# Performance work log

Hardware: AMD Instinct MI355X
Metric: run time of the kernel (lower is better)

The kernel has to match this reference:

```python
import jax, jax.numpy as jnp
import numpy as np

N_NODES = 50000
N_EDGES = 800000
D_IN = 64
D_OUT = 64
EPS = 0.0  # DGL GINConv default init_eps=0, not learnable


def setup_inputs() -> dict:
    key = jax.random.key(0)
    k1, k2, k3, k4, k5 = jax.random.split(key, 5)
    node_inputs = jax.random.normal(k1, (N_NODES, D_IN), dtype=jnp.float32)
    src = jax.random.randint(k2, (N_EDGES,), 0, N_NODES, dtype=jnp.int64)
    dst = jax.random.randint(k3, (N_EDGES,), 0, N_NODES, dtype=jnp.int64)
    # nn.Linear(in_feats, out_feats) params (PyTorch layout: W [out, in])
    bound = 1.0 / np.sqrt(D_IN)
    W = jax.random.uniform(k4, (D_OUT, D_IN), dtype=jnp.float32, minval=-bound, maxval=bound)
    b = jax.random.uniform(k5, (D_OUT,), dtype=jnp.float32, minval=-bound, maxval=bound)
    return {"node_inputs": node_inputs, "W": W, "b": b, "src": src, "dst": dst}


def reference(node_inputs, W, b, src, dst):
    # GIN sum aggregation: for each node, sum features of in-neighbors
    # messages: [E, D_IN] gathered, scatter-summed into [N, D_IN]
    agg = jax.ops.segment_sum(node_inputs[src], dst, num_segments=N_NODES)
    h = (1.0 + EPS) * node_inputs + agg          # [N, D_IN]
    h = h @ W.T + b                              # Linear -> [N, D_OUT]
    h = jnp.tanh(h)
    # Dropout is identity in eval mode (deterministic reference)
    return h
```

## Files before the change

kernel.cpp:

```cpp
#include <hip/hip_runtime.h>

#define N_NODES 50000
#define N_EDGES 800000
#define D 64

#define NBIN 512
#define BINW 98
#define PBLK 160
#define EPB  5000
#define CAPB 26
#define NCAP 64
#define WGROUP 260

typedef int iv4 __attribute__((ext_vector_type(4)));

__global__ __launch_bounds__(512) void gin_part(const int* __restrict__ src,
                                                const int* __restrict__ dst,
                                                unsigned int* __restrict__ regions,
                                                int* __restrict__ bincnt) {
    __shared__ int lcnt[NBIN];
    const int tid = threadIdx.x;
    if (tid < NBIN) lcnt[tid] = 0;
    __syncthreads();

    const int ebase = blockIdx.x * EPB;
    unsigned int* __restrict__ rbase = regions + (size_t)blockIdx.x * NBIN * CAPB;

    for (int i = tid; i < EPB / 4; i += 512) {
        const int e = ebase + i * 4;
        const iv4 d4 = *(const iv4*)&dst[e];
        const iv4 s4 = *(const iv4*)&src[e];
        const int dd[4] = {d4.x, d4.y, d4.z, d4.w};
        const int ss[4] = {s4.x, s4.y, s4.z, s4.w};
        #pragma unroll
        for (int j = 0; j < 4; ++j) {
            const int bin = dd[j] / BINW;
            const int pos = atomicAdd(&lcnt[bin], 1);
            if (pos < CAPB)
                rbase[bin * CAPB + pos] = ((unsigned)dd[j] << 16) | (unsigned)ss[j];
        }
    }
    __syncthreads();
    if (tid < NBIN) bincnt[blockIdx.x * NBIN + tid] = lcnt[tid] < CAPB ? lcnt[tid] : CAPB;
}

__device__ __forceinline__ float fast_tanh(float v) {
    return 1.0f - 2.0f / (__expf(2.0f * v) + 1.0f);
}

__global__ __launch_bounds__(1024) void gin_node(const float* __restrict__ x,
                                                 const float* __restrict__ W,
                                                 const float* __restrict__ bias,
                                                 const unsigned int* __restrict__ regions,
                                                 const int* __restrict__ bincnt,
                                                 float* __restrict__ out) {
    __shared__ unsigned short sbuck[BINW * NCAP];
    __shared__ int   lcnt[BINW];
    __shared__ float Wt2[16 * WGROUP];
    __shared__ float hs[16][68];

    const int tid  = threadIdx.x;
    const int lane = tid & 63;
    const int wv   = tid >> 6;
    const int b    = blockIdx.x;
    const int lo   = b * BINW;

    if (tid < BINW) lcnt[tid] = 0;
    #pragma unroll
    for (int i = tid; i < D * D; i += 1024) {
        const int f = i >> 6, k = i & 63;
        Wt2[(k >> 2) * WGROUP + (f << 2) + (k & 3)] = W[i];
    }
    __syncthreads();

    for (int pb = wv; pb < PBLK; pb += 16) {
        const int n = bincnt[pb * NBIN + b];
        if (lane < n) {
            const unsigned e = regions[((size_t)pb * NBIN + b) * CAPB + lane];
            const int dl  = (int)(e >> 16) - lo;
            const int pos = atomicAdd(&lcnt[dl], 1);
            if (pos < NCAP) sbuck[dl * NCAP + pos] = (unsigned short)(e & 0xffffu);
        }
    }
    __syncthreads();

    const float bf = bias[lane];
    for (int li = wv; li < BINW; li += 16) {
        const int node = lo + li;
        if (node >= N_NODES) break;
        int cn = lcnt[li]; if (cn > NCAP) cn = NCAP;
        const int sid = (int)sbuck[li * NCAP + lane];

        float a0 = x[(size_t)node * D + lane];
        float a1 = 0.f, a2 = 0.f, a3 = 0.f, a4 = 0.f, a5 = 0.f, a6 = 0.f, a7 = 0.f;
        for (int i = 0; i < cn; i += 8) {
            int i0 = __shfl(sid, i + 0), i1 = __shfl(sid, i + 1);
            int i2 = __shfl(sid, i + 2), i3 = __shfl(sid, i + 3);
            int i4 = __shfl(sid, i + 4), i5 = __shfl(sid, i + 5);
            int i6 = __shfl(sid, i + 6), i7 = __shfl(sid, i + 7);
            const int rem = cn - i;
            i0 = (0 < rem) ? i0 : 0;  i1 = (1 < rem) ? i1 : 0;
            i2 = (2 < rem) ? i2 : 0;  i3 = (3 < rem) ? i3 : 0;
            i4 = (4 < rem) ? i4 : 0;  i5 = (5 < rem) ? i5 : 0;
            i6 = (6 < rem) ? i6 : 0;  i7 = (7 < rem) ? i7 : 0;
            const float v0 = x[(size_t)i0 * D + lane], v1 = x[(size_t)i1 * D + lane];
            const float v2 = x[(size_t)i2 * D + lane], v3 = x[(size_t)i3 * D + lane];
            const float v4 = x[(size_t)i4 * D + lane], v5 = x[(size_t)i5 * D + lane];
            const float v6 = x[(size_t)i6 * D + lane], v7 = x[(size_t)i7 * D + lane];
            a0 += (0 < rem) ? v0 : 0.f;  a1 += (1 < rem) ? v1 : 0.f;
            a2 += (2 < rem) ? v2 : 0.f;  a3 += (3 < rem) ? v3 : 0.f;
            a4 += (4 < rem) ? v4 : 0.f;  a5 += (5 < rem) ? v5 : 0.f;
            a6 += (6 < rem) ? v6 : 0.f;  a7 += (7 < rem) ? v7 : 0.f;
        }
        hs[wv][lane] = ((a0 + a1) + (a2 + a3)) + ((a4 + a5) + (a6 + a7));

        float r0 = bf, r1 = 0.f, r2 = 0.f, r3 = 0.f;
        #pragma unroll
        for (int kg = 0; kg < 16; ++kg) {
            const float4 w  = *(const float4*)&Wt2[kg * WGROUP + (lane << 2)];
            const float4 hv = *(const float4*)&hs[wv][kg << 2];
            r0 += hv.x * w.x;
            r1 += hv.y * w.y;
            r2 += hv.z * w.z;
            r3 += hv.w * w.w;
        }
        out[(size_t)node * D + lane] = fast_tanh((r0 + r1) + (r2 + r3));
    }
}

extern "C" void kernel_launch(void* const* d_in, const int* in_sizes, int n_in,
                              void* d_out, int out_size, void* d_ws, size_t ws_size,
                              hipStream_t stream) {
    const float* x    = (const float*)d_in[0];
    const float* W    = (const float*)d_in[1];
    const float* bias = (const float*)d_in[2];
    const int*   src  = (const int*)d_in[3];
    const int*   dst  = (const int*)d_in[4];
    float*       out  = (float*)d_out;

    unsigned int* regions = (unsigned int*)d_ws;
    int*          bincnt  = (int*)(regions + (size_t)PBLK * NBIN * CAPB);

    gin_part<<<PBLK, 512, 0, stream>>>(src, dst, regions, bincnt);
    gin_node<<<NBIN, 1024, 0, stream>>>(x, W, bias, regions, bincnt, out);
}
```

Baseline: 125.9 us.

## Aggregate four nodes per wavefront with float4 gathers and pair partition reads

Each wavefront now handles four nodes at once, with 16 lanes per node gathering neighbour rows as float4 loads, reading source ids straight from LDS instead of through shuffles. Nodes are split into contiguous chunks per wave, and the following matvec loops over the four staged rows. The partition-read phase also lets each wave read two partition bins at once using 32-lane halves, since bins hold at most 26 entries. This widens per-lane loads and cuts idle lanes in the gather, at the cost of a serial per-node matvec loop and more complex bounds handling.

```diff
diff --git a/kernel.cpp b/kernel.cpp
--- a/kernel.cpp
+++ b/kernel.cpp
@@ -57,11 +57,13 @@
     __shared__ unsigned short sbuck[BINW * NCAP];
     __shared__ int   lcnt[BINW];
     __shared__ float Wt2[16 * WGROUP];
-    __shared__ float hs[16][68];
+    __shared__ float hs[16][4][68];
 
     const int tid  = threadIdx.x;
     const int lane = tid & 63;
     const int wv   = tid >> 6;
+    const int sub  = lane >> 4;
+    const int q    = lane & 15;
     const int b    = blockIdx.x;
     const int lo   = b * BINW;
 
@@ -73,10 +75,13 @@
     }
     __syncthreads();
 
-    for (int pb = wv; pb < PBLK; pb += 16) {
+    const int g2 = lane >> 5;
+    const int l2 = lane & 31;
+    for (int p2 = wv; p2 < PBLK / 2; p2 += 16) {
+        const int pb = p2 * 2 + g2;
         const int n = bincnt[pb * NBIN + b];
-        if (lane < n) {
-            const unsigned e = regions[((size_t)pb * NBIN + b) * CAPB + lane];
+        if (l2 < n) {
+            const unsigned e = regions[((size_t)pb * NBIN + b) * CAPB + l2];
             const int dl  = (int)(e >> 16) - lo;
             const int pos = atomicAdd(&lcnt[dl], 1);
             if (pos < NCAP) sbuck[dl * NCAP + pos] = (unsigned short)(e & 0xffffu);
@@ -85,46 +90,66 @@
     __syncthreads();
 
     const float bf = bias[lane];
-    for (int li = wv; li < BINW; li += 16) {
-        const int node = lo + li;
-        if (node >= N_NODES) break;
-        int cn = lcnt[li]; if (cn > NCAP) cn = NCAP;
-        const int sid = (int)sbuck[li * NCAP + lane];
+    const int ncnt   = (wv < 2) ? 7 : 6;
+    const int nstart = wv * 6 + ((wv < 2) ? wv : 2);
+    const int nend   = nstart + ncnt;
 
-        float a0 = x[(size_t)node * D + lane];
-        float a1 = 0.f, a2 = 0.f, a3 = 0.f, a4 = 0.f, a5 = 0.f, a6 = 0.f, a7 = 0.f;
-        for (int i = 0; i < cn; i += 8) {
-            int i0 = __shfl(sid, i + 0), i1 = __shfl(sid, i + 1);
-            int i2 = __shfl(sid, i + 2), i3 = __shfl(sid, i + 3);
-            int i4 = __shfl(sid, i + 4), i5 = __shfl(sid, i + 5);
-            int i6 = __shfl(sid, i + 6), i7 = __shfl(sid, i + 7);
+    for (int base = nstart; base < nend; base += 4) {
+        const int li    = base + sub;
+        const bool nv   = (li < nend);
+        const int  liC  = nv ? li : (nend - 1);
+        const int  node = lo + liC;
+        const bool ndv  = nv && (node < N_NODES);
+        const int  nodeC = (node < N_NODES) ? node : (N_NODES - 1);
+        int cn = ndv ? lcnt[liC] : 0;
+        if (cn > NCAP) cn = NCAP;
+
+        float4 acc = *(const float4*)&x[(size_t)nodeC * D + (q << 2)];
+
+        const unsigned short* __restrict__ sl = &sbuck[liC * NCAP];
+        for (int i = 0; i < cn; i += 4) {
             const int rem = cn - i;
-            i0 = (0 < rem) ? i0 : 0;  i1 = (1 < rem) ? i1 : 0;
-            i2 = (2 < rem) ? i2 : 0;  i3 = (3 < rem) ? i3 : 0;
-            i4 = (4 < rem) ? i4 : 0;  i5 = (5 < rem) ? i5 : 0;
-            i6 = (6 < rem) ? i6 : 0;  i7 = (7 < rem) ? i7 : 0;
-            const float v0 = x[(size_t)i0 * D + lane], v1 = x[(size_t)i1 * D + lane];
-            const float v2 = x[(size_t)i2 * D + lane], v3 = x[(size_t)i3 * D + lane];
-            const float v4 = x[(size_t)i4 * D + lane], v5 = x[(size_t)i5 * D + lane];
-            const float v6 = x[(size_t)i6 * D + lane], v7 = x[(size_t)i7 * D + lane];
-            a0 += (0 < rem) ? v0 : 0.f;  a1 += (1 < rem) ? v1 : 0.f;
-            a2 += (2 < rem) ? v2 : 0.f;  a3 += (3 < rem) ? v3 : 0.f;
-            a4 += (4 < rem) ? v4 : 0.f;  a5 += (5 < rem) ? v5 : 0.f;
-            a6 += (6 < rem) ? v6 : 0.f;  a7 += (7 < rem) ? v7 : 0.f;
+            int s0 = (int)sl[i];
+            int s1 = (int)sl[(i + 1) & (NCAP - 1)];
+            int s2 = (int)sl[(i + 2) & (NCAP - 1)];
+            int s3 = (int)sl[(i + 3) & (NCAP - 1)];
+            s1 = (1 < rem) ? s1 : 0;
+            s2 = (2 < rem) ? s2 : 0;
+            s3 = (3 < rem) ? s3 : 0;
+            const float4 v0 = *(const float4*)&x[(size_t)s0 * D + (q << 2)];
+            const float4 v1 = *(const float4*)&x[(size_t)s1 * D + (q << 2)];
+            const float4 v2 = *(const float4*)&x[(size_t)s2 * D + (q << 2)];
+            const float4 v3 = *(const float4*)&x[(size_t)s3 * D + (q << 2)];
+            const float m1 = (1 < rem) ? 1.f : 0.f;
+            const float m2 = (2 < rem) ? 1.f : 0.f;
+            const float m3 = (3 < rem) ? 1.f : 0.f;
+            acc.x += v0.x; acc.y += v0.y; acc.z += v0.z; acc.w += v0.w;
+            acc.x = fmaf(v1.x, m1, acc.x); acc.y = fmaf(v1.y, m1, acc.y);
+            acc.z = fmaf(v1.z, m1, acc.z); acc.w = fmaf(v1.w, m1, acc.w);
+            acc.x = fmaf(v2.x, m2, acc.x); acc.y = fmaf(v2.y, m2, acc.y);
+            acc.z = fmaf(v2.z, m2, acc.z); acc.w = fmaf(v2.w, m2, acc.w);
+            acc.x = fmaf(v3.x, m3, acc.x); acc.y = fmaf(v3.y, m3, acc.y);
+            acc.z = fmaf(v3.z, m3, acc.z); acc.w = fmaf(v3.w, m3, acc.w);
         }
-        hs[wv][lane] = ((a0 + a1) + (a2 + a3)) + ((a4 + a5) + (a6 + a7));
+        *(float4*)&hs[wv][sub][q << 2] = acc;
 
-        float r0 = bf, r1 = 0.f, r2 = 0.f, r3 = 0.f;
-        #pragma unroll
-        for (int kg = 0; kg < 16; ++kg) {
-            const float4 w  = *(const float4*)&Wt2[kg * WGROUP + (lane << 2)];
-            const float4 hv = *(const float4*)&hs[wv][kg << 2];
-            r0 += hv.x * w.x;
-            r1 += hv.y * w.y;
-            r2 += hv.z * w.z;
-            r3 += hv.w * w.w;
+        const int left = nend - base;
+        const int mcnt = left < 4 ? left : 4;
+        for (int j = 0; j < mcnt; ++j) {
+            const int nodej = lo + base + j;
+            if (nodej >= N_NODES) break;
+            float r0 = bf, r1 = 0.f, r2 = 0.f, r3 = 0.f;
+            #pragma unroll
+            for (int kg = 0; kg < 16; ++kg) {
+                const float4 w  = *(const float4*)&Wt2[kg * WGROUP + (lane << 2)];
+                const float4 hv = *(const float4*)&hs[wv][j][kg << 2];
+                r0 += hv.x * w.x;
+                r1 += hv.y * w.y;
+                r2 += hv.z * w.z;
+                r3 += hv.w * w.w;
+            }
+            out[(size_t)nodej * D + lane] = fast_tanh((r0 + r1) + (r2 + r3));
         }
-        out[(size_t)node * D + lane] = fast_tanh((r0 + r1) + (r2 + r3));
     }
 }
 
```

After: 119.1 us. 1.06x faster.
